# Optimization experiments

Measured on AMD Instinct MI355X. Metric: run time of the kernel, lower is better.

## Reference

```python
import jax, jax.numpy as jnp
import numpy as np

N, E, D, L, G = 50000, 640000, 128, 5, 128
BN_EPS = 1e-5

def _bn(x, g, b):
    # training-mode batchnorm over axis 0, biased variance (torch semantics)
    m = x.mean(axis=0)
    v = x.var(axis=0)
    return (x - m) * jax.lax.rsqrt(v + BN_EPS) * g + b

def setup_inputs():
    key = jax.random.key(0)
    ks = iter(jax.random.split(key, 40))
    rn = lambda shape, s=0.05: jax.random.normal(next(ks), shape, jnp.float32) * s
    inp = {}
    inp['x'] = jax.random.randint(next(ks), (N, 1), 0, 300)
    inp['edge_index'] = jax.random.randint(next(ks), (2, E), 0, N)
    inp['edge_attr'] = jax.random.normal(next(ks), (E, 7), jnp.float32)
    inp['batch'] = jnp.sort(jax.random.randint(next(ks), (N,), 0, G))
    inp['node_emb'] = rn((300, D))
    inp['vn_emb'] = jnp.zeros((1, D), jnp.float32)
    inp['eps'] = jnp.zeros((L,), jnp.float32)
    inp['edge_W'] = rn((L, 7, D)); inp['edge_b'] = rn((L, D))
    inp['W1'] = rn((L, D, 2 * D)); inp['b1'] = rn((L, 2 * D))
    inp['bn1_g'] = 1.0 + rn((L, 2 * D)); inp['bn1_b'] = rn((L, 2 * D))
    inp['W2'] = rn((L, 2 * D, D)); inp['b2'] = rn((L, D))
    inp['bn_g'] = 1.0 + rn((L, D)); inp['bn_b'] = rn((L, D))
    inp['vn_W1'] = rn((L - 1, D, 2 * D)); inp['vn_b1'] = rn((L - 1, 2 * D))
    inp['vn_bn1_g'] = 1.0 + rn((L - 1, 2 * D)); inp['vn_bn1_b'] = rn((L - 1, 2 * D))
    inp['vn_W2'] = rn((L - 1, 2 * D, D)); inp['vn_b2'] = rn((L - 1, D))
    inp['vn_bn2_g'] = 1.0 + rn((L - 1, D)); inp['vn_bn2_b'] = rn((L - 1, D))
    return inp

def reference(x, edge_index, edge_attr, batch, node_emb, vn_emb, eps,
              edge_W, edge_b, W1, b1, bn1_g, bn1_b, W2, b2, bn_g, bn_b,
              vn_W1, vn_b1, vn_bn1_g, vn_bn1_b, vn_W2, vn_b2, vn_bn2_g, vn_bn2_b):
    src, dst = edge_index[0], edge_index[1]
    h = node_emb[x[:, 0]]                      # [N, D]
    vn = jnp.broadcast_to(vn_emb, (G, D))      # virtualnode state per graph
    for l in range(L):
        h_in = h + vn[batch]                   # virtualnode broadcast
        e = edge_attr @ edge_W[l] + edge_b[l]  # [E, D]
        msg = jax.nn.relu(h_in[src] + e)       # gather + fused elementwise
        agg = jax.ops.segment_sum(msg, dst, num_segments=N)
        z = (1.0 + eps[l]) * h_in + agg
        z = jax.nn.relu(_bn(z @ W1[l] + b1[l], bn1_g[l], bn1_b[l]))
        z = _bn(z @ W2[l] + b2[l], bn_g[l], bn_b[l])
        h_out = jax.nn.relu(z) if l != L - 1 else z
        if l < L - 1:
            pooled = jax.ops.segment_sum(h_in, batch, num_segments=G)
            v = vn + pooled
            v = jax.nn.relu(_bn(v @ vn_W1[l] + vn_b1[l], vn_bn1_g[l], vn_bn1_b[l]))
            vn = jax.nn.relu(_bn(v @ vn_W2[l] + vn_b2[l], vn_bn2_g[l], vn_bn2_b[l]))
        h = h_out
    return h
```

## Files before the change

### kernel.cpp

```cpp
#include <hip/hip_runtime.h>
#include <stdint.h>

#define NN 50000
#define EE 640000
#define DD 128
#define LL 5
#define GG 128
#define D2 256

using bf16x8 = __attribute__((ext_vector_type(8))) short;
using f32x4v = __attribute__((ext_vector_type(4))) float;
using u32x4v = __attribute__((ext_vector_type(4))) unsigned int;

__device__ __forceinline__ unsigned short f2bf(float f){
  union { float f; uint32_t u; } c; c.f = f;
  uint32_t u = c.u;
  uint32_t r = (u + 0x7FFFu + ((u >> 16) & 1u)) >> 16;
  return (unsigned short)r;
}


__global__ __launch_bounds__(256) void zero_kernel(float* p, int n){
  int i = blockIdx.x*256 + threadIdx.x;
  if (i < n) p[i] = 0.f;
}

__global__ __launch_bounds__(256) void count_kernel(const int* __restrict__ ei, int* __restrict__ counts){
  int e = blockIdx.x*256 + threadIdx.x;
  if (e < EE) atomicAdd(&counts[ei[EE + e]], 1);
}

#define SCAN_B 512
__global__ __launch_bounds__(SCAN_B) void scan1_kernel(const int* __restrict__ counts, int* __restrict__ bsums, int n){
  __shared__ int sh[SCAN_B];
  int b = blockIdx.x, t = threadIdx.x;
  int i = b*SCAN_B + t;
  sh[t] = (i < n) ? counts[i] : 0;
  __syncthreads();
  for (int s = SCAN_B/2; s > 0; s >>= 1){
    if (t < s) sh[t] += sh[t+s];
    __syncthreads();
  }
  if (t == 0) bsums[b] = sh[0];
}

__global__ void scan2_kernel(int* bsums, int nb){
  if (threadIdx.x == 0){
    int run = 0;
    for (int i = 0; i < nb; ++i){ int v = bsums[i]; bsums[i] = run; run += v; }
  }
}

__global__ __launch_bounds__(SCAN_B) void scan3_kernel(const int* __restrict__ counts, const int* __restrict__ bsums,
                                                       int* __restrict__ startp, int* __restrict__ cursor, int n){
  __shared__ int sh[SCAN_B];
  int b = blockIdx.x, t = threadIdx.x;
  int i = b*SCAN_B + t;
  int v = (i < n) ? counts[i] : 0;
  sh[t] = v;
  __syncthreads();
  for (int s = 1; s < SCAN_B; s <<= 1){
    int add = (t >= s) ? sh[t-s] : 0;
    __syncthreads();
    sh[t] += add;
    __syncthreads();
  }
  int excl = sh[t] - v + bsums[b];
  if (i < n){ startp[i] = excl; cursor[i] = excl; }
  if (i == n-1) startp[n] = excl + v;
}

__global__ __launch_bounds__(256) void fill_kernel(const int* __restrict__ ei, int* __restrict__ cursor, int* __restrict__ csr){
  int e = blockIdx.x*256 + threadIdx.x;
  if (e < EE){
    int d = ei[EE + e];
    int slot = atomicAdd(&cursor[d], 1);
    csr[slot] = e;
  }
}

__global__ __launch_bounds__(256) void embed_kernel(const int* __restrict__ x, const float* __restrict__ emb, float* __restrict__ h){
  int idx = blockIdx.x*256 + threadIdx.x;
  if (idx >= NN*32) return;
  int i = idx >> 5, c4 = idx & 31;
  int xi = x[i];
  *(f32x4v*)(h + (size_t)idx*4) = *(const f32x4v*)(emb + ((size_t)xi*32 + c4)*4);
}

__global__ __launch_bounds__(256) void vninit_kernel(const float* __restrict__ vn_emb, float* __restrict__ vn){
  int idx = blockIdx.x*256 + threadIdx.x;
  if (idx >= GG*32) return;
  *(f32x4v*)(vn + (size_t)idx*4) = *(const f32x4v*)(vn_emb + (size_t)(idx & 31)*4);
}

__global__ __launch_bounds__(256) void wtrans_kernel(const float* __restrict__ W1, const float* __restrict__ W2,
                                                     unsigned short* __restrict__ W1T, unsigned short* __restrict__ W2T){
  int idx = blockIdx.x*256 + threadIdx.x;
  const int total = LL*DD*D2;
  if (idx < total){
    int l = idx / (DD*D2);
    int rem = idx - l*(DD*D2);
    int k = rem / D2;
    int c = rem - k*D2;
    W1T[(size_t)l*32768 + (size_t)c*128 + k] = f2bf(W1[idx]);
  } else if (idx < 2*total){
    int j = idx - total;
    int l = j / (DD*D2);
    int rem = j - l*(DD*D2);
    int k = rem / DD;
    int c = rem - k*DD;
    W2T[(size_t)l*32768 + (size_t)c*256 + k] = f2bf(W2[j]);
  }
}


__global__ __launch_bounds__(256) void hin_kernel(const float* __restrict__ h, const float* __restrict__ vn,
                                                  const int* __restrict__ batch, float* __restrict__ hin){
  int idx = blockIdx.x*256 + threadIdx.x;
  if (idx >= NN*32) return;
  int i = idx >> 5, c4 = idx & 31;
  int b = batch[i];
  f32x4v hv = *(const f32x4v*)(h + (size_t)idx*4);
  f32x4v vv = *(const f32x4v*)(vn + ((size_t)b*32 + c4)*4);
  *(f32x4v*)(hin + (size_t)idx*4) = hv + vv;
}

__global__ __launch_bounds__(128) void agg_kernel(const float* __restrict__ hin, const int* __restrict__ csr,
                                                  const int* __restrict__ startp, const int* __restrict__ ei,
                                                  const float* __restrict__ ea, const float* __restrict__ eW,
                                                  const float* __restrict__ eb, const float* __restrict__ eps, int l,
                                                  unsigned short* __restrict__ zout){
  int node = blockIdx.x, d = threadIdx.x;
  int s0 = startp[node], s1 = startp[node+1];
  float w[7];
  #pragma unroll
  for (int k = 0; k < 7; ++k) w[k] = eW[k*128 + d];
  float bd = eb[d];
  float acc = 0.f;
  __shared__ int eids[32];
  __shared__ int srcs[32];
  __shared__ float eav[32][8];
  for (int base = s0; base < s1; base += 32){
    int cnt = min(32, s1 - base);
    __syncthreads();
    if (d < cnt){ int e = csr[base + d]; eids[d] = e; srcs[d] = ei[e]; }
    __syncthreads();
    for (int q = d; q < cnt*7; q += 128){
      int j = q / 7, k = q - j*7;
      eav[j][k] = ea[(size_t)eids[j]*7 + k];
    }
    __syncthreads();
    for (int j = 0; j < cnt; ++j){
      float hv = hin[(size_t)srcs[j]*128 + d];
      float e = bd;
      #pragma unroll
      for (int k = 0; k < 7; ++k) e += eav[j][k]*w[k];
      float m = hv + e;
      acc += (m > 0.f) ? m : 0.f;
    }
  }
  float one = 1.f + eps[l];
  float z = one*hin[(size_t)node*128 + d] + acc;
  zout[(size_t)node*128 + d] = f2bf(z);
}

__global__ __launch_bounds__(256) void gemm1_kernel(const unsigned short* __restrict__ A,
                                                    const unsigned short* __restrict__ BT,
                                                    const float* __restrict__ bias,
                                                    float* __restrict__ Y,
                                                    float* __restrict__ sums, float* __restrict__ sqs){
  __shared__ __align__(16) unsigned short Al[128*128];
  __shared__ __align__(16) unsigned short Bl[128*128];
  const int t = threadIdx.x;
  const int rb = blockIdx.x, cb = blockIdx.y;
  for (int it = 0; it < 8; ++it){
    int idx = it*256 + t;
    int row = idx >> 4, ch = idx & 15;
    int grow = rb*128 + row;
    u32x4v v = {0,0,0,0};
    if (grow < NN) v = *(const u32x4v*)(A + (size_t)grow*128 + ch*8);
    *(u32x4v*)((char*)Al + row*256 + ((ch*16) ^ ((row&7)<<4))) = v;
  }
  for (int it = 0; it < 8; ++it){
    int idx = it*256 + t;
    int row = idx >> 4, ch = idx & 15;
    u32x4v v = *(const u32x4v*)(BT + (size_t)(cb*128 + row)*128 + ch*8);
    *(u32x4v*)((char*)Bl + row*256 + ((ch*16) ^ ((row&7)<<4))) = v;
  }
  __syncthreads();
  const int lane = t & 63, wave = t >> 6;
  const int wm = wave >> 1, wn = wave & 1;
  const int r0 = lane & 15, kg = lane >> 4;
  f32x4v acc[4][4] = {};
  #pragma unroll
  for (int kk = 0; kk < 4; ++kk){
    const int kb = kk*64 + kg*16;
    bf16x8 a[4], b[4];
    #pragma unroll
    for (int m = 0; m < 4; ++m){
      int row = wm*64 + m*16 + r0;
      a[m] = *(const bf16x8*)((const char*)Al + row*256 + (kb ^ ((r0&7)<<4)));
    }
    #pragma unroll
    for (int n = 0; n < 4; ++n){
      int col = wn*64 + n*16 + r0;
      b[n] = *(const bf16x8*)((const char*)Bl + col*256 + (kb ^ ((r0&7)<<4)));
    }
    #pragma unroll
    for (int m = 0; m < 4; ++m)
      #pragma unroll
      for (int n = 0; n < 4; ++n)
        acc[m][n] = __builtin_amdgcn_mfma_f32_16x16x32_bf16(a[m], b[n], acc[m][n], 0, 0, 0);
  }
  #pragma unroll
  for (int n = 0; n < 4; ++n){
    const int col = cb*128 + wn*64 + n*16 + r0;
    const float bv = bias[col];
    float s = 0.f, q = 0.f;
    #pragma unroll
    for (int m = 0; m < 4; ++m){
      const int rowb = rb*128 + wm*64 + m*16 + kg*4;
      #pragma unroll
      for (int j = 0; j < 4; ++j){
        int grow = rowb + j;
        if (grow < NN){
          float v = acc[m][n][j] + bv;
          Y[(size_t)grow*256 + col] = v;
          s += v; q += v*v;
        }
      }
    }
    s += __shfl_xor(s, 16); q += __shfl_xor(q, 16);
    s += __shfl_xor(s, 32); q += __shfl_xor(q, 32);
    if (kg == 0){ atomicAdd(&sums[col], s); atomicAdd(&sqs[col], q); }
  }
}

__global__ __launch_bounds__(256) void gemm2_kernel(const float* __restrict__ Yin,
                                                    const float* __restrict__ scl, const float* __restrict__ shf,
                                                    const unsigned short* __restrict__ BT,
                                                    const float* __restrict__ bias,
                                                    float* __restrict__ Y,
                                                    float* __restrict__ sums, float* __restrict__ sqs){
  __shared__ __align__(16) unsigned short Al[128*128];
  __shared__ __align__(16) unsigned short Bl[128*128];
  __shared__ float s_scl[256], s_shf[256];
  const int t = threadIdx.x;
  const int rb = blockIdx.x;
  if (t < 256){ s_scl[t] = scl[t]; s_shf[t] = shf[t]; }
  const int lane = t & 63, wave = t >> 6;
  const int wm = wave >> 1, wn = wave & 1;
  const int r0 = lane & 15, kg = lane >> 4;
  f32x4v acc[4][4] = {};
  for (int kt = 0; kt < 2; ++kt){
    __syncthreads();
    for (int it = 0; it < 8; ++it){
      int idx = it*256 + t;
      int row = idx >> 4, ch = idx & 15;
      int grow = rb*128 + row;
      int c0 = kt*128 + ch*8;
      u32x4v pv = {0,0,0,0};
      if (grow < NN){
        f32x4v ya = *(const f32x4v*)(Yin + (size_t)grow*256 + c0);
        f32x4v yb = *(const f32x4v*)(Yin + (size_t)grow*256 + c0 + 4);
        unsigned short tb[8];
        #pragma unroll
        for (int jj = 0; jj < 4; ++jj){
          float a = ya[jj]*s_scl[c0+jj] + s_shf[c0+jj];
          tb[jj] = f2bf(a > 0.f ? a : 0.f);
        }
        #pragma unroll
        for (int jj = 0; jj < 4; ++jj){
          float a = yb[jj]*s_scl[c0+4+jj] + s_shf[c0+4+jj];
          tb[4+jj] = f2bf(a > 0.f ? a : 0.f);
        }
        pv[0] = (uint32_t)tb[0] | ((uint32_t)tb[1] << 16);
        pv[1] = (uint32_t)tb[2] | ((uint32_t)tb[3] << 16);
        pv[2] = (uint32_t)tb[4] | ((uint32_t)tb[5] << 16);
        pv[3] = (uint32_t)tb[6] | ((uint32_t)tb[7] << 16);
      }
      *(u32x4v*)((char*)Al + row*256 + ((ch*16) ^ ((row&7)<<4))) = pv;
    }
    for (int it = 0; it < 8; ++it){
      int idx = it*256 + t;
      int row = idx >> 4, ch = idx & 15;
      u32x4v v = *(const u32x4v*)(BT + (size_t)row*256 + kt*128 + ch*8);
      *(u32x4v*)((char*)Bl + row*256 + ((ch*16) ^ ((row&7)<<4))) = v;
    }
    __syncthreads();
    #pragma unroll
    for (int kk = 0; kk < 4; ++kk){
      const int kb = kk*64 + kg*16;
      bf16x8 a[4], b[4];
      #pragma unroll
      for (int m = 0; m < 4; ++m){
        int row = wm*64 + m*16 + r0;
        a[m] = *(const bf16x8*)((const char*)Al + row*256 + (kb ^ ((r0&7)<<4)));
      }
      #pragma unroll
      for (int n = 0; n < 4; ++n){
        int col = wn*64 + n*16 + r0;
        b[n] = *(const bf16x8*)((const char*)Bl + col*256 + (kb ^ ((r0&7)<<4)));
      }
      #pragma unroll
      for (int m = 0; m < 4; ++m)
        #pragma unroll
        for (int n = 0; n < 4; ++n)
          acc[m][n] = __builtin_amdgcn_mfma_f32_16x16x32_bf16(a[m], b[n], acc[m][n], 0, 0, 0);
    }
  }
  #pragma unroll
  for (int n = 0; n < 4; ++n){
    const int col = wn*64 + n*16 + r0;
    const float bv = bias[col];
    float s = 0.f, q = 0.f;
    #pragma unroll
    for (int m = 0; m < 4; ++m){
      const int rowb = rb*128 + wm*64 + m*16 + kg*4;
      #pragma unroll
      for (int j = 0; j < 4; ++j){
        int grow = rowb + j;
        if (grow < NN){
          float v = acc[m][n][j] + bv;
          Y[(size_t)grow*128 + col] = v;
          s += v; q += v*v;
        }
      }
    }
    s += __shfl_xor(s, 16); q += __shfl_xor(q, 16);
    s += __shfl_xor(s, 32); q += __shfl_xor(q, 32);
    if (kg == 0){ atomicAdd(&sums[col], s); atomicAdd(&sqs[col], q); }
  }
}

__global__ void bnfin_kernel(const float* __restrict__ sums, const float* __restrict__ sqs,
                             const float* __restrict__ g, const float* __restrict__ b,
                             float* __restrict__ scl, float* __restrict__ shf, int C, float invcnt){
  int c = blockIdx.x*blockDim.x + threadIdx.x;
  if (c < C){
    float m = sums[c]*invcnt;
    float v = sqs[c]*invcnt - m*m;
    v = v > 0.f ? v : 0.f;
    float inv = rsqrtf(v + 1e-5f);
    float s = g[c]*inv;
    scl[c] = s;
    shf[c] = b[c] - m*s;
  }
}

__global__ __launch_bounds__(256) void happly_kernel(const float* __restrict__ y2, const float* __restrict__ scl,
                                                     const float* __restrict__ shf, float* __restrict__ h, int relu){
  int idx = blockIdx.x*256 + threadIdx.x;
  if (idx >= NN*32) return;
  int c4 = idx & 31;
  f32x4v y = *(const f32x4v*)(y2 + (size_t)idx*4);
  f32x4v s = *(const f32x4v*)(scl + (size_t)c4*4);
  f32x4v t = *(const f32x4v*)(shf + (size_t)c4*4);
  f32x4v o;
  #pragma unroll
  for (int j = 0; j < 4; ++j){
    float v = y[j]*s[j] + t[j];
    o[j] = (relu && v < 0.f) ? 0.f : v;
  }
  *(f32x4v*)(h + (size_t)idx*4) = o;
}

__global__ __launch_bounds__(256) void vcopy_kernel(const float* __restrict__ vn, float* __restrict__ vbuf){
  int idx = blockIdx.x*256 + threadIdx.x;
  if (idx < GG*DD) vbuf[idx] = vn[idx];
}

#define POOL_ROWS 128
__global__ __launch_bounds__(128) void pool2_kernel(const float* __restrict__ hin, const int* __restrict__ batch,
                                                    float* __restrict__ vout){
  int r0 = blockIdx.x*POOL_ROWS;
  int r1 = r0 + POOL_ROWS; if (r1 > NN) r1 = NN;
  int d = threadIdx.x;
  __shared__ int sb[POOL_ROWS];
  if (r0 + d < r1) sb[d] = batch[r0 + d];
  __syncthreads();
  int curg = sb[0];
  float acc = 0.f;
  for (int r = r0; r < r1; ++r){
    int g = sb[r - r0];
    if (g != curg){
      atomicAdd(&vout[(size_t)curg*DD + d], acc);
      acc = 0.f; curg = g;
    }
    acc += hin[(size_t)r*DD + d];
  }
  atomicAdd(&vout[(size_t)curg*DD + d], acc);
}

__global__ __launch_bounds__(256) void vmlp1_kernel(const float* __restrict__ V, const float* __restrict__ W,
                                                    const float* __restrict__ bias, float* __restrict__ Yo,
                                                    float* __restrict__ sums, float* __restrict__ sqs){
  __shared__ float vrow[128];
  int r = blockIdx.x, c = threadIdx.x;
  if (c < 128) vrow[c] = V[r*128 + c];
  __syncthreads();
  float acc = 0.f;
  #pragma unroll 8
  for (int k = 0; k < 128; ++k) acc += vrow[k]*W[k*256 + c];
  float y = acc + bias[c];
  Yo[r*256 + c] = y;
  atomicAdd(&sums[c], y);
  atomicAdd(&sqs[c], y*y);
}

__global__ __launch_bounds__(128) void vmlp2_kernel(const float* __restrict__ Yin, const float* __restrict__ scl,
                                                    const float* __restrict__ shf, const float* __restrict__ W,
                                                    const float* __restrict__ bias, float* __restrict__ Yo,
                                                    float* __restrict__ sums, float* __restrict__ sqs){
  __shared__ float arow[256];
  int r = blockIdx.x, c = threadIdx.x;
  for (int k = c; k < 256; k += 128){
    float a = Yin[r*256 + k]*scl[k] + shf[k];
    arow[k] = a > 0.f ? a : 0.f;
  }
  __syncthreads();
  float acc = 0.f;
  #pragma unroll 8
  for (int k = 0; k < 256; ++k) acc += arow[k]*W[k*128 + c];
  float y = acc + bias[c];
  Yo[r*128 + c] = y;
  atomicAdd(&sums[c], y);
  atomicAdd(&sqs[c], y*y);
}

__global__ __launch_bounds__(256) void va_kernel(const float* __restrict__ yv2, const float* __restrict__ scl,
                                                 const float* __restrict__ shf, float* __restrict__ vn){
  int idx = blockIdx.x*256 + threadIdx.x;
  if (idx < GG*128){
    int c = idx & 127;
    float v = yv2[idx]*scl[c] + shf[c];
    vn[idx] = v > 0.f ? v : 0.f;
  }
}


extern "C" void kernel_launch(void* const* d_in, const int* in_sizes, int n_in,
                              void* d_out, int out_size, void* d_ws, size_t ws_size,
                              hipStream_t stream){
  const int*   x         = (const int*)  d_in[0];
  const int*   ei        = (const int*)  d_in[1];
  const float* edge_attr = (const float*)d_in[2];
  const int*   batch     = (const int*)  d_in[3];
  const float* node_emb  = (const float*)d_in[4];
  const float* vn_emb    = (const float*)d_in[5];
  const float* eps       = (const float*)d_in[6];
  const float* edge_W    = (const float*)d_in[7];
  const float* edge_b    = (const float*)d_in[8];
  const float* W1        = (const float*)d_in[9];
  const float* b1        = (const float*)d_in[10];
  const float* bn1_g     = (const float*)d_in[11];
  const float* bn1_b     = (const float*)d_in[12];
  const float* W2        = (const float*)d_in[13];
  const float* b2        = (const float*)d_in[14];
  const float* bn_g      = (const float*)d_in[15];
  const float* bn_b      = (const float*)d_in[16];
  const float* vn_W1     = (const float*)d_in[17];
  const float* vn_b1     = (const float*)d_in[18];
  const float* vn_bn1_g  = (const float*)d_in[19];
  const float* vn_bn1_b  = (const float*)d_in[20];
  const float* vn_W2     = (const float*)d_in[21];
  const float* vn_b2     = (const float*)d_in[22];
  const float* vn_bn2_g  = (const float*)d_in[23];
  const float* vn_bn2_b  = (const float*)d_in[24];
  float* h = (float*)d_out;

  char* ws = (char*)d_ws;
  size_t off = 0;
  auto alloc = [&](size_t bytes)->char*{
    char* p = ws + off; off += (bytes + 255) & ~(size_t)255; return p;
  };
  float*          hin    = (float*)         alloc((size_t)NN*DD*4);
  float*          y1     = (float*)         alloc((size_t)NN*D2*4);
  float*          y2     = (float*)         alloc((size_t)NN*DD*4);
  unsigned short* zbuf   = (unsigned short*)alloc((size_t)NN*DD*2);
  float*          vn     = (float*)         alloc((size_t)GG*DD*4);
  float*          vbuf   = (float*)         alloc((size_t)GG*DD*4);
  float*          yv1    = (float*)         alloc((size_t)GG*D2*4);
  float*          yv2    = (float*)         alloc((size_t)GG*DD*4);
  unsigned short* W1T    = (unsigned short*)alloc((size_t)LL*D2*DD*2);
  unsigned short* W2T    = (unsigned short*)alloc((size_t)LL*D2*DD*2);
  float*          stats  = (float*)         alloc(16*256*4);
  int*            counts = (int*)           alloc((size_t)NN*4);
  int*            startp = (int*)           alloc((size_t)(NN+1)*4);
  int*            cursor = (int*)           alloc((size_t)NN*4);
  int*            csr    = (int*)           alloc((size_t)EE*4);
  int*            bsums  = (int*)           alloc(128*4);

  float* sum1 = stats + 0*256,  *sq1 = stats + 1*256,  *scale1 = stats + 2*256,  *shift1 = stats + 3*256;
  float* sum2 = stats + 4*256,  *sq2 = stats + 5*256,  *scale2 = stats + 6*256,  *shift2 = stats + 7*256;
  float* sumv1= stats + 8*256,  *sqv1= stats + 9*256,  *scalev1= stats + 10*256, *shiftv1= stats + 11*256;
  float* sumv2= stats + 12*256, *sqv2= stats + 13*256, *scalev2= stats + 14*256, *shiftv2= stats + 15*256;

  const int nb_scan = (NN + SCAN_B - 1)/SCAN_B;
  const int ew_blocks = (NN*32 + 255)/256;
  const int pool_blocks = (NN + POOL_ROWS - 1)/POOL_ROWS;

  zero_kernel<<<(NN+255)/256, 256, 0, stream>>>((float*)counts, NN);
  count_kernel<<<EE/256, 256, 0, stream>>>(ei, counts);
  scan1_kernel<<<nb_scan, SCAN_B, 0, stream>>>(counts, bsums, NN);
  scan2_kernel<<<1, 64, 0, stream>>>(bsums, nb_scan);
  scan3_kernel<<<nb_scan, SCAN_B, 0, stream>>>(counts, bsums, startp, cursor, NN);
  fill_kernel<<<EE/256, 256, 0, stream>>>(ei, cursor, csr);
  embed_kernel<<<ew_blocks, 256, 0, stream>>>(x, node_emb, h);
  vninit_kernel<<<(GG*32 + 255)/256, 256, 0, stream>>>(vn_emb, vn);
  wtrans_kernel<<<(2*LL*DD*D2 + 255)/256, 256, 0, stream>>>(W1, W2, W1T, W2T);

  for (int l = 0; l < LL; ++l){
    zero_kernel<<<16, 256, 0, stream>>>(stats, 16*256);
    hin_kernel<<<ew_blocks, 256, 0, stream>>>(h, vn, batch, hin);
    agg_kernel<<<NN, 128, 0, stream>>>(hin, csr, startp, ei, edge_attr,
                                       edge_W + (size_t)l*7*DD, edge_b + (size_t)l*DD, eps, l, zbuf);
    gemm1_kernel<<<dim3((NN+127)/128, 2), 256, 0, stream>>>(zbuf, W1T + (size_t)l*32768,
                                                            b1 + (size_t)l*D2, y1, sum1, sq1);
    bnfin_kernel<<<1, 256, 0, stream>>>(sum1, sq1, bn1_g + (size_t)l*D2, bn1_b + (size_t)l*D2,
                                        scale1, shift1, D2, 1.f/(float)NN);
    gemm2_kernel<<<(NN+127)/128, 256, 0, stream>>>(y1, scale1, shift1, W2T + (size_t)l*32768,
                                                   b2 + (size_t)l*DD, y2, sum2, sq2);
    bnfin_kernel<<<1, 256, 0, stream>>>(sum2, sq2, bn_g + (size_t)l*DD, bn_b + (size_t)l*DD,
                                        scale2, shift2, DD, 1.f/(float)NN);
    happly_kernel<<<ew_blocks, 256, 0, stream>>>(y2, scale2, shift2, h, (l != LL-1) ? 1 : 0);
    if (l < LL-1){
      vcopy_kernel<<<(GG*DD + 255)/256, 256, 0, stream>>>(vn, vbuf);
      pool2_kernel<<<pool_blocks, 128, 0, stream>>>(hin, batch, vbuf);
      vmlp1_kernel<<<GG, 256, 0, stream>>>(vbuf, vn_W1 + (size_t)l*DD*D2, vn_b1 + (size_t)l*D2,
                                           yv1, sumv1, sqv1);
      bnfin_kernel<<<1, 256, 0, stream>>>(sumv1, sqv1, vn_bn1_g + (size_t)l*D2, vn_bn1_b + (size_t)l*D2,
                                          scalev1, shiftv1, D2, 1.f/(float)GG);
      vmlp2_kernel<<<GG, 128, 0, stream>>>(yv1, scalev1, shiftv1, vn_W2 + (size_t)l*D2*DD,
                                           vn_b2 + (size_t)l*DD, yv2, sumv2, sqv2);
      bnfin_kernel<<<1, 256, 0, stream>>>(sumv2, sqv2, vn_bn2_g + (size_t)l*DD, vn_bn2_b + (size_t)l*DD,
                                          scalev2, shiftv2, DD, 1.f/(float)GG);
      va_kernel<<<(GG*DD + 255)/256, 256, 0, stream>>>(yv2, scalev2, shiftv2, vn);
    }
  }
  (void)in_sizes; (void)n_in; (void)out_size; (void)ws_size;
}
```

Baseline: 1.374 ms.

## Fuse layer epilogues, store activations in bf16, and presort edge data by destination

Pre-gathers edge sources and padded edge attributes into destination-sorted CSR order so aggregation reads them contiguously. Node states and intermediate activations (hin, y1, y2) are stored in bf16 instead of fp32, roughly halving traffic in gather, GEMM and elementwise passes. Batchnorm finalisation is folded into consumer kernels, and the h-apply, virtual-node add and pooling steps are fused into one per-layer kernel, with per-layer stats zeroed once up front. This cuts kernel launches and memory passes at the cost of extra bf16 rounding and a reordering of when the virtual node is updated relative to pooling.

```diff
diff --git a/kernel.cpp b/kernel.cpp
--- a/kernel.cpp
+++ b/kernel.cpp
@@ -17,6 +17,9 @@
   uint32_t u = c.u;
   uint32_t r = (u + 0x7FFFu + ((u >> 16) & 1u)) >> 16;
   return (unsigned short)r;
+}
+__device__ __forceinline__ float bf2f(unsigned short u){
+  union { uint32_t u; float f; } c; c.u = ((uint32_t)u) << 16; return c.f;
 }
 
 
@@ -79,18 +82,20 @@
   }
 }
 
-__global__ __launch_bounds__(256) void embed_kernel(const int* __restrict__ x, const float* __restrict__ emb, float* __restrict__ h){
-  int idx = blockIdx.x*256 + threadIdx.x;
-  if (idx >= NN*32) return;
-  int i = idx >> 5, c4 = idx & 31;
-  int xi = x[i];
-  *(f32x4v*)(h + (size_t)idx*4) = *(const f32x4v*)(emb + ((size_t)xi*32 + c4)*4);
-}
-
-__global__ __launch_bounds__(256) void vninit_kernel(const float* __restrict__ vn_emb, float* __restrict__ vn){
-  int idx = blockIdx.x*256 + threadIdx.x;
-  if (idx >= GG*32) return;
-  *(f32x4v*)(vn + (size_t)idx*4) = *(const f32x4v*)(vn_emb + (size_t)(idx & 31)*4);
+__global__ __launch_bounds__(256) void egather_kernel(const int* __restrict__ csr, const int* __restrict__ ei,
+                                                      const float* __restrict__ ea,
+                                                      int* __restrict__ csr_src, float* __restrict__ csr_ea8){
+  int s = blockIdx.x*256 + threadIdx.x;
+  if (s < EE){
+    int e = csr[s];
+    csr_src[s] = ei[e];
+    float v[8];
+    #pragma unroll
+    for (int k = 0; k < 7; ++k) v[k] = ea[(size_t)e*7 + k];
+    v[7] = 0.f;
+    #pragma unroll
+    for (int k = 0; k < 8; ++k) csr_ea8[(size_t)s*8 + k] = v[k];
+  }
 }
 
 __global__ __launch_bounds__(256) void wtrans_kernel(const float* __restrict__ W1, const float* __restrict__ W2,
@@ -113,23 +118,43 @@
   }
 }
 
-
-__global__ __launch_bounds__(256) void hin_kernel(const float* __restrict__ h, const float* __restrict__ vn,
-                                                  const int* __restrict__ batch, float* __restrict__ hin){
-  int idx = blockIdx.x*256 + threadIdx.x;
-  if (idx >= NN*32) return;
-  int i = idx >> 5, c4 = idx & 31;
-  int b = batch[i];
-  f32x4v hv = *(const f32x4v*)(h + (size_t)idx*4);
-  f32x4v vv = *(const f32x4v*)(vn + ((size_t)b*32 + c4)*4);
-  *(f32x4v*)(hin + (size_t)idx*4) = hv + vv;
-}
-
-__global__ __launch_bounds__(128) void agg_kernel(const float* __restrict__ hin, const int* __restrict__ csr,
-                                                  const int* __restrict__ startp, const int* __restrict__ ei,
-                                                  const float* __restrict__ ea, const float* __restrict__ eW,
-                                                  const float* __restrict__ eb, const float* __restrict__ eps, int l,
-                                                  unsigned short* __restrict__ zout){
+__global__ __launch_bounds__(128) void init_kernel(const int* __restrict__ x, const int* __restrict__ batch,
+                                                   const float* __restrict__ emb, const float* __restrict__ vn_emb,
+                                                   unsigned short* __restrict__ hin_bf, float* __restrict__ vbuf0,
+                                                   float* __restrict__ vn){
+  int r0 = blockIdx.x*128;
+  int r1 = r0 + 128; if (r1 > NN) r1 = NN;
+  int d = threadIdx.x;
+  float ve = vn_emb[d];
+  if (blockIdx.x == 0){
+    for (int g = 0; g < GG; ++g) vn[(size_t)g*DD + d] = ve;
+  }
+  __shared__ int sb[128];
+  __shared__ int sx[128];
+  if (r0 + d < r1){ sb[d] = batch[r0 + d]; sx[d] = x[r0 + d]; }
+  __syncthreads();
+  int curg = sb[0];
+  float pacc = 0.f;
+  for (int r = r0; r < r1; ++r){
+    int g = sb[r - r0];
+    if (g != curg){
+      atomicAdd(&vbuf0[(size_t)curg*DD + d], pacc);
+      pacc = 0.f; curg = g;
+    }
+    float hv = emb[(size_t)sx[r - r0]*DD + d] + ve;
+    hin_bf[(size_t)r*DD + d] = f2bf(hv);
+    pacc += hv;
+  }
+  atomicAdd(&vbuf0[(size_t)curg*DD + d], pacc);
+}
+
+
+__global__ __launch_bounds__(128) void agg2_kernel(const unsigned short* __restrict__ hin_bf,
+                                                   const int* __restrict__ csr_src, const float* __restrict__ csr_ea8,
+                                                   const int* __restrict__ startp,
+                                                   const float* __restrict__ eW, const float* __restrict__ eb,
+                                                   const float* __restrict__ eps, int l,
+                                                   unsigned short* __restrict__ zout){
   int node = blockIdx.x, d = threadIdx.x;
   int s0 = startp[node], s1 = startp[node+1];
   float w[7];
@@ -137,37 +162,34 @@
   for (int k = 0; k < 7; ++k) w[k] = eW[k*128 + d];
   float bd = eb[d];
   float acc = 0.f;
-  __shared__ int eids[32];
-  __shared__ int srcs[32];
-  __shared__ float eav[32][8];
+  __shared__ int ssrc[32];
+  __shared__ float sattr[32][8];
   for (int base = s0; base < s1; base += 32){
     int cnt = min(32, s1 - base);
     __syncthreads();
-    if (d < cnt){ int e = csr[base + d]; eids[d] = e; srcs[d] = ei[e]; }
-    __syncthreads();
-    for (int q = d; q < cnt*7; q += 128){
-      int j = q / 7, k = q - j*7;
-      eav[j][k] = ea[(size_t)eids[j]*7 + k];
+    if (d < cnt) ssrc[d] = csr_src[base + d];
+    for (int q = d; q < cnt*8; q += 128){
+      sattr[q >> 3][q & 7] = csr_ea8[(size_t)base*8 + q];
     }
     __syncthreads();
     for (int j = 0; j < cnt; ++j){
-      float hv = hin[(size_t)srcs[j]*128 + d];
+      float hv = bf2f(hin_bf[(size_t)ssrc[j]*128 + d]);
       float e = bd;
       #pragma unroll
-      for (int k = 0; k < 7; ++k) e += eav[j][k]*w[k];
+      for (int k = 0; k < 7; ++k) e += sattr[j][k]*w[k];
       float m = hv + e;
       acc += (m > 0.f) ? m : 0.f;
     }
   }
   float one = 1.f + eps[l];
-  float z = one*hin[(size_t)node*128 + d] + acc;
+  float z = one*bf2f(hin_bf[(size_t)node*128 + d]) + acc;
   zout[(size_t)node*128 + d] = f2bf(z);
 }
 
 __global__ __launch_bounds__(256) void gemm1_kernel(const unsigned short* __restrict__ A,
                                                     const unsigned short* __restrict__ BT,
                                                     const float* __restrict__ bias,
-                                                    float* __restrict__ Y,
+                                                    unsigned short* __restrict__ Y,
                                                     float* __restrict__ sums, float* __restrict__ sqs){
   __shared__ __align__(16) unsigned short Al[128*128];
   __shared__ __align__(16) unsigned short Bl[128*128];
@@ -225,7 +247,7 @@
         int grow = rowb + j;
         if (grow < NN){
           float v = acc[m][n][j] + bv;
-          Y[(size_t)grow*256 + col] = v;
+          Y[(size_t)grow*256 + col] = f2bf(v);
           s += v; q += v*v;
         }
       }
@@ -236,18 +258,28 @@
   }
 }
 
-__global__ __launch_bounds__(256) void gemm2_kernel(const float* __restrict__ Yin,
-                                                    const float* __restrict__ scl, const float* __restrict__ shf,
+template<int FINAL>
+__global__ __launch_bounds__(256) void gemm2_kernel(const unsigned short* __restrict__ Yin,
+                                                    const float* __restrict__ sum1, const float* __restrict__ sq1,
+                                                    const float* __restrict__ bg, const float* __restrict__ bb,
                                                     const unsigned short* __restrict__ BT,
                                                     const float* __restrict__ bias,
-                                                    float* __restrict__ Y,
+                                                    unsigned short* __restrict__ Yh, float* __restrict__ Yf,
                                                     float* __restrict__ sums, float* __restrict__ sqs){
   __shared__ __align__(16) unsigned short Al[128*128];
   __shared__ __align__(16) unsigned short Bl[128*128];
   __shared__ float s_scl[256], s_shf[256];
   const int t = threadIdx.x;
   const int rb = blockIdx.x;
-  if (t < 256){ s_scl[t] = scl[t]; s_shf[t] = shf[t]; }
+  {
+    const float invn = 1.f/(float)NN;
+    float m = sum1[t]*invn;
+    float var = sq1[t]*invn - m*m;
+    var = var > 0.f ? var : 0.f;
+    float sc = bg[t]*rsqrtf(var + 1e-5f);
+    s_scl[t] = sc;
+    s_shf[t] = bb[t] - m*sc;
+  }
   const int lane = t & 63, wave = t >> 6;
   const int wm = wave >> 1, wn = wave & 1;
   const int r0 = lane & 15, kg = lane >> 4;
@@ -261,18 +293,17 @@
       int c0 = kt*128 + ch*8;
       u32x4v pv = {0,0,0,0};
       if (grow < NN){
-        f32x4v ya = *(const f32x4v*)(Yin + (size_t)grow*256 + c0);
-        f32x4v yb = *(const f32x4v*)(Yin + (size_t)grow*256 + c0 + 4);
+        u32x4v yv = *(const u32x4v*)(Yin + (size_t)grow*256 + c0);
         unsigned short tb[8];
         #pragma unroll
         for (int jj = 0; jj < 4; ++jj){
-          float a = ya[jj]*s_scl[c0+jj] + s_shf[c0+jj];
-          tb[jj] = f2bf(a > 0.f ? a : 0.f);
-        }
-        #pragma unroll
-        for (int jj = 0; jj < 4; ++jj){
-          float a = yb[jj]*s_scl[c0+4+jj] + s_shf[c0+4+jj];
-          tb[4+jj] = f2bf(a > 0.f ? a : 0.f);
+          uint32_t pw = yv[jj];
+          float a0 = bf2f((unsigned short)(pw & 0xFFFFu));
+          float a1 = bf2f((unsigned short)(pw >> 16));
+          float v0 = a0*s_scl[c0 + 2*jj]     + s_shf[c0 + 2*jj];
+          float v1 = a1*s_scl[c0 + 2*jj + 1] + s_shf[c0 + 2*jj + 1];
+          tb[2*jj]     = f2bf(v0 > 0.f ? v0 : 0.f);
+          tb[2*jj + 1] = f2bf(v1 > 0.f ? v1 : 0.f);
         }
         pv[0] = (uint32_t)tb[0] | ((uint32_t)tb[1] << 16);
         pv[1] = (uint32_t)tb[2] | ((uint32_t)tb[3] << 16);
@@ -322,7 +353,8 @@
         int grow = rowb + j;
         if (grow < NN){
           float v = acc[m][n][j] + bv;
-          Y[(size_t)grow*128 + col] = v;
+          if (FINAL) Yf[(size_t)grow*128 + col] = v;
+          else       Yh[(size_t)grow*128 + col] = f2bf(v);
           s += v; q += v*v;
         }
       }
@@ -333,71 +365,71 @@
   }
 }
 
-__global__ void bnfin_kernel(const float* __restrict__ sums, const float* __restrict__ sqs,
-                             const float* __restrict__ g, const float* __restrict__ b,
-                             float* __restrict__ scl, float* __restrict__ shf, int C, float invcnt){
-  int c = blockIdx.x*blockDim.x + threadIdx.x;
-  if (c < C){
-    float m = sums[c]*invcnt;
-    float v = sqs[c]*invcnt - m*m;
+__global__ __launch_bounds__(128) void happly_fused_kernel(const unsigned short* __restrict__ y2h,
+                                                           const float* __restrict__ sum2, const float* __restrict__ sq2,
+                                                           const float* __restrict__ bg, const float* __restrict__ bb,
+                                                           const float* __restrict__ vn, const int* __restrict__ batch,
+                                                           unsigned short* __restrict__ hin_bf, float* __restrict__ vbuf_next){
+  int r0 = blockIdx.x*128;
+  int r1 = r0 + 128; if (r1 > NN) r1 = NN;
+  int d = threadIdx.x;
+  const float invn = 1.f/(float)NN;
+  float m = sum2[d]*invn;
+  float var = sq2[d]*invn - m*m;
+  var = var > 0.f ? var : 0.f;
+  float sc = bg[d]*rsqrtf(var + 1e-5f);
+  float sh = bb[d] - m*sc;
+  __shared__ int sb[128];
+  if (r0 + d < r1) sb[d] = batch[r0 + d];
+  __syncthreads();
+  int curg = sb[0];
+  float vnv = vn[(size_t)curg*DD + d];
+  float pacc = 0.f;
+  for (int r = r0; r < r1; ++r){
+    int g = sb[r - r0];
+    if (g != curg){
+      atomicAdd(&vbuf_next[(size_t)curg*DD + d], pacc);
+      pacc = 0.f; curg = g;
+      vnv = vn[(size_t)curg*DD + d];
+    }
+    float y = bf2f(y2h[(size_t)r*DD + d]);
+    float v = y*sc + sh;
     v = v > 0.f ? v : 0.f;
-    float inv = rsqrtf(v + 1e-5f);
-    float s = g[c]*inv;
-    scl[c] = s;
-    shf[c] = b[c] - m*s;
-  }
-}
-
-__global__ __launch_bounds__(256) void happly_kernel(const float* __restrict__ y2, const float* __restrict__ scl,
-                                                     const float* __restrict__ shf, float* __restrict__ h, int relu){
+    float hv = v + vnv;
+    hin_bf[(size_t)r*DD + d] = f2bf(hv);
+    pacc += hv;
+  }
+  atomicAdd(&vbuf_next[(size_t)curg*DD + d], pacc);
+}
+
+__global__ __launch_bounds__(256) void happly_final_kernel(float* __restrict__ y,
+                                                           const float* __restrict__ sum2, const float* __restrict__ sq2,
+                                                           const float* __restrict__ bg, const float* __restrict__ bb){
   int idx = blockIdx.x*256 + threadIdx.x;
   if (idx >= NN*32) return;
   int c4 = idx & 31;
-  f32x4v y = *(const f32x4v*)(y2 + (size_t)idx*4);
-  f32x4v s = *(const f32x4v*)(scl + (size_t)c4*4);
-  f32x4v t = *(const f32x4v*)(shf + (size_t)c4*4);
+  const float invn = 1.f/(float)NN;
+  f32x4v yv = *(const f32x4v*)(y + (size_t)idx*4);
   f32x4v o;
   #pragma unroll
   for (int j = 0; j < 4; ++j){
-    float v = y[j]*s[j] + t[j];
-    o[j] = (relu && v < 0.f) ? 0.f : v;
-  }
-  *(f32x4v*)(h + (size_t)idx*4) = o;
-}
-
-__global__ __launch_bounds__(256) void vcopy_kernel(const float* __restrict__ vn, float* __restrict__ vbuf){
-  int idx = blockIdx.x*256 + threadIdx.x;
-  if (idx < GG*DD) vbuf[idx] = vn[idx];
-}
-
-#define POOL_ROWS 128
-__global__ __launch_bounds__(128) void pool2_kernel(const float* __restrict__ hin, const int* __restrict__ batch,
-                                                    float* __restrict__ vout){
-  int r0 = blockIdx.x*POOL_ROWS;
-  int r1 = r0 + POOL_ROWS; if (r1 > NN) r1 = NN;
-  int d = threadIdx.x;
-  __shared__ int sb[POOL_ROWS];
-  if (r0 + d < r1) sb[d] = batch[r0 + d];
-  __syncthreads();
-  int curg = sb[0];
-  float acc = 0.f;
-  for (int r = r0; r < r1; ++r){
-    int g = sb[r - r0];
-    if (g != curg){
-      atomicAdd(&vout[(size_t)curg*DD + d], acc);
-      acc = 0.f; curg = g;
-    }
-    acc += hin[(size_t)r*DD + d];
-  }
-  atomicAdd(&vout[(size_t)curg*DD + d], acc);
-}
-
-__global__ __launch_bounds__(256) void vmlp1_kernel(const float* __restrict__ V, const float* __restrict__ W,
-                                                    const float* __restrict__ bias, float* __restrict__ Yo,
+    int c = c4*4 + j;
+    float m = sum2[c]*invn;
+    float var = sq2[c]*invn - m*m;
+    var = var > 0.f ? var : 0.f;
+    float sc = bg[c]*rsqrtf(var + 1e-5f);
+    o[j] = (yv[j] - m)*sc + bb[c];
+  }
+  *(f32x4v*)(y + (size_t)idx*4) = o;
+}
+
+__global__ __launch_bounds__(256) void vmlp1_kernel(const float* __restrict__ vn, const float* __restrict__ vbufl,
+                                                    const float* __restrict__ W, const float* __restrict__ bias,
+                                                    float* __restrict__ Yo,
                                                     float* __restrict__ sums, float* __restrict__ sqs){
   __shared__ float vrow[128];
   int r = blockIdx.x, c = threadIdx.x;
-  if (c < 128) vrow[c] = V[r*128 + c];
+  if (c < 128) vrow[c] = vn[r*128 + c] + vbufl[r*128 + c];
   __syncthreads();
   float acc = 0.f;
   #pragma unroll 8
@@ -408,14 +440,27 @@
   atomicAdd(&sqs[c], y*y);
 }
 
-__global__ __launch_bounds__(128) void vmlp2_kernel(const float* __restrict__ Yin, const float* __restrict__ scl,
-                                                    const float* __restrict__ shf, const float* __restrict__ W,
-                                                    const float* __restrict__ bias, float* __restrict__ Yo,
+__global__ __launch_bounds__(128) void vmlp2_kernel(const float* __restrict__ Yin,
+                                                    const float* __restrict__ sumv1, const float* __restrict__ sqv1,
+                                                    const float* __restrict__ vg, const float* __restrict__ vb,
+                                                    const float* __restrict__ W, const float* __restrict__ bias,
+                                                    float* __restrict__ Yo,
                                                     float* __restrict__ sums, float* __restrict__ sqs){
   __shared__ float arow[256];
+  __shared__ float s_scl[256], s_shf[256];
   int r = blockIdx.x, c = threadIdx.x;
+  const float invg = 1.f/(float)GG;
   for (int k = c; k < 256; k += 128){
-    float a = Yin[r*256 + k]*scl[k] + shf[k];
+    float m = sumv1[k]*invg;
+    float var = sqv1[k]*invg - m*m;
+    var = var > 0.f ? var : 0.f;
+    float sc = vg[k]*rsqrtf(var + 1e-5f);
+    s_scl[k] = sc;
+    s_shf[k] = vb[k] - m*sc;
+  }
+  __syncthreads();
+  for (int k = c; k < 256; k += 128){
+    float a = Yin[r*256 + k]*s_scl[k] + s_shf[k];
     arow[k] = a > 0.f ? a : 0.f;
   }
   __syncthreads();
@@ -428,12 +473,19 @@
   atomicAdd(&sqs[c], y*y);
 }
 
-__global__ __launch_bounds__(256) void va_kernel(const float* __restrict__ yv2, const float* __restrict__ scl,
-                                                 const float* __restrict__ shf, float* __restrict__ vn){
+__global__ __launch_bounds__(256) void va_kernel(const float* __restrict__ yv2,
+                                                 const float* __restrict__ sumv2, const float* __restrict__ sqv2,
+                                                 const float* __restrict__ vg, const float* __restrict__ vb,
+                                                 float* __restrict__ vn){
   int idx = blockIdx.x*256 + threadIdx.x;
   if (idx < GG*128){
     int c = idx & 127;
-    float v = yv2[idx]*scl[c] + shf[c];
+    const float invg = 1.f/(float)GG;
+    float m = sumv2[c]*invg;
+    float var = sqv2[c]*invg - m*m;
+    var = var > 0.f ? var : 0.f;
+    float sc = vg[c]*rsqrtf(var + 1e-5f);
+    float v = (yv2[idx] - m)*sc + vb[c];
     vn[idx] = v > 0.f ? v : 0.f;
   }
 }
@@ -467,75 +519,85 @@
   const float* vn_b2     = (const float*)d_in[22];
   const float* vn_bn2_g  = (const float*)d_in[23];
   const float* vn_bn2_b  = (const float*)d_in[24];
-  float* h = (float*)d_out;
+  float* hout = (float*)d_out;
 
   char* ws = (char*)d_ws;
   size_t off = 0;
   auto alloc = [&](size_t bytes)->char*{
     char* p = ws + off; off += (bytes + 255) & ~(size_t)255; return p;
   };
-  float*          hin    = (float*)         alloc((size_t)NN*DD*4);
-  float*          y1     = (float*)         alloc((size_t)NN*D2*4);
-  float*          y2     = (float*)         alloc((size_t)NN*DD*4);
-  unsigned short* zbuf   = (unsigned short*)alloc((size_t)NN*DD*2);
+  unsigned short* hin_bf = (unsigned short*)alloc((size_t)NN*DD*2);
+  unsigned short* zy     = (unsigned short*)alloc((size_t)NN*DD*2);
+  unsigned short* y1h    = (unsigned short*)alloc((size_t)NN*D2*2);
   float*          vn     = (float*)         alloc((size_t)GG*DD*4);
-  float*          vbuf   = (float*)         alloc((size_t)GG*DD*4);
   float*          yv1    = (float*)         alloc((size_t)GG*D2*4);
   float*          yv2    = (float*)         alloc((size_t)GG*DD*4);
   unsigned short* W1T    = (unsigned short*)alloc((size_t)LL*D2*DD*2);
   unsigned short* W2T    = (unsigned short*)alloc((size_t)LL*D2*DD*2);
-  float*          stats  = (float*)         alloc(16*256*4);
-  int*            counts = (int*)           alloc((size_t)NN*4);
-  int*            startp = (int*)           alloc((size_t)(NN+1)*4);
-  int*            cursor = (int*)           alloc((size_t)NN*4);
-  int*            csr    = (int*)           alloc((size_t)EE*4);
-  int*            bsums  = (int*)           alloc(128*4);
-
-  float* sum1 = stats + 0*256,  *sq1 = stats + 1*256,  *scale1 = stats + 2*256,  *shift1 = stats + 3*256;
-  float* sum2 = stats + 4*256,  *sq2 = stats + 5*256,  *scale2 = stats + 6*256,  *shift2 = stats + 7*256;
-  float* sumv1= stats + 8*256,  *sqv1= stats + 9*256,  *scalev1= stats + 10*256, *shiftv1= stats + 11*256;
-  float* sumv2= stats + 12*256, *sqv2= stats + 13*256, *scalev2= stats + 14*256, *shiftv2= stats + 15*256;
+  const int STATS_F = LL*8*256;
+  const int VBUF_F  = 5*GG*DD;
+  const int ZTOT    = STATS_F + VBUF_F + NN;
+  float* zeroreg = (float*)alloc((size_t)ZTOT*4);
+  float* stats_all = zeroreg;
+  float* vbuf_all  = zeroreg + STATS_F;
+  int*   counts    = (int*)(zeroreg + STATS_F + VBUF_F);
+  int*   startp = (int*)  alloc((size_t)(NN+1)*4);
+  int*   cursor = (int*)  alloc((size_t)NN*4);
+  int*   csr    = (int*)  alloc((size_t)EE*4);
+  int*   bsums  = (int*)  alloc(128*4);
+  int*   csr_src= (int*)  alloc((size_t)EE*4);
+  float* csr_ea8= (float*)alloc((size_t)EE*8*4);
 
   const int nb_scan = (NN + SCAN_B - 1)/SCAN_B;
+  const int row_blocks = (NN + 127)/128;
   const int ew_blocks = (NN*32 + 255)/256;
-  const int pool_blocks = (NN + POOL_ROWS - 1)/POOL_ROWS;
-
-  zero_kernel<<<(NN+255)/256, 256, 0, stream>>>((float*)counts, NN);
+
+  zero_kernel<<<(ZTOT + 255)/256, 256, 0, stream>>>(zeroreg, ZTOT);
   count_kernel<<<EE/256, 256, 0, stream>>>(ei, counts);
   scan1_kernel<<<nb_scan, SCAN_B, 0, stream>>>(counts, bsums, NN);
   scan2_kernel<<<1, 64, 0, stream>>>(bsums, nb_scan);
   scan3_kernel<<<nb_scan, SCAN_B, 0, stream>>>(counts, bsums, startp, cursor, NN);
   fill_kernel<<<EE/256, 256, 0, stream>>>(ei, cursor, csr);
-  embed_kernel<<<ew_blocks, 256, 0, stream>>>(x, node_emb, h);
-  vninit_kernel<<<(GG*32 + 255)/256, 256, 0, stream>>>(vn_emb, vn);
+  egather_kernel<<<EE/256, 256, 0, stream>>>(csr, ei, edge_attr, csr_src, csr_ea8);
   wtrans_kernel<<<(2*LL*DD*D2 + 255)/256, 256, 0, stream>>>(W1, W2, W1T, W2T);
+  init_kernel<<<row_blocks, 128, 0, stream>>>(x, batch, node_emb, vn_emb, hin_bf, vbuf_all, vn);
 
   for (int l = 0; l < LL; ++l){
-    zero_kernel<<<16, 256, 0, stream>>>(stats, 16*256);
-    hin_kernel<<<ew_blocks, 256, 0, stream>>>(h, vn, batch, hin);
-    agg_kernel<<<NN, 128, 0, stream>>>(hin, csr, startp, ei, edge_attr,
-                                       edge_W + (size_t)l*7*DD, edge_b + (size_t)l*DD, eps, l, zbuf);
-    gemm1_kernel<<<dim3((NN+127)/128, 2), 256, 0, stream>>>(zbuf, W1T + (size_t)l*32768,
-                                                            b1 + (size_t)l*D2, y1, sum1, sq1);
-    bnfin_kernel<<<1, 256, 0, stream>>>(sum1, sq1, bn1_g + (size_t)l*D2, bn1_b + (size_t)l*D2,
-                                        scale1, shift1, D2, 1.f/(float)NN);
-    gemm2_kernel<<<(NN+127)/128, 256, 0, stream>>>(y1, scale1, shift1, W2T + (size_t)l*32768,
-                                                   b2 + (size_t)l*DD, y2, sum2, sq2);
-    bnfin_kernel<<<1, 256, 0, stream>>>(sum2, sq2, bn_g + (size_t)l*DD, bn_b + (size_t)l*DD,
-                                        scale2, shift2, DD, 1.f/(float)NN);
-    happly_kernel<<<ew_blocks, 256, 0, stream>>>(y2, scale2, shift2, h, (l != LL-1) ? 1 : 0);
-    if (l < LL-1){
-      vcopy_kernel<<<(GG*DD + 255)/256, 256, 0, stream>>>(vn, vbuf);
-      pool2_kernel<<<pool_blocks, 128, 0, stream>>>(hin, batch, vbuf);
-      vmlp1_kernel<<<GG, 256, 0, stream>>>(vbuf, vn_W1 + (size_t)l*DD*D2, vn_b1 + (size_t)l*D2,
+    float* st    = stats_all + (size_t)l*8*256;
+    float* sum1  = st + 0*256, *sq1  = st + 1*256;
+    float* sum2  = st + 2*256, *sq2  = st + 3*256;
+    float* sumv1 = st + 4*256, *sqv1 = st + 5*256;
+    float* sumv2 = st + 6*256, *sqv2 = st + 7*256;
+
+    agg2_kernel<<<NN, 128, 0, stream>>>(hin_bf, csr_src, csr_ea8, startp,
+                                        edge_W + (size_t)l*7*DD, edge_b + (size_t)l*DD, eps, l, zy);
+    gemm1_kernel<<<dim3(row_blocks, 2), 256, 0, stream>>>(zy, W1T + (size_t)l*32768,
+                                                          b1 + (size_t)l*D2, y1h, sum1, sq1);
+    if (l != LL-1){
+      gemm2_kernel<0><<<row_blocks, 256, 0, stream>>>(y1h, sum1, sq1,
+                                                      bn1_g + (size_t)l*D2, bn1_b + (size_t)l*D2,
+                                                      W2T + (size_t)l*32768, b2 + (size_t)l*DD,
+                                                      zy, nullptr, sum2, sq2);
+      float* vbufl = vbuf_all + (size_t)l*GG*DD;
+      float* vbufn = vbuf_all + (size_t)(l+1)*GG*DD;
+      vmlp1_kernel<<<GG, 256, 0, stream>>>(vn, vbufl, vn_W1 + (size_t)l*DD*D2, vn_b1 + (size_t)l*D2,
                                            yv1, sumv1, sqv1);
-      bnfin_kernel<<<1, 256, 0, stream>>>(sumv1, sqv1, vn_bn1_g + (size_t)l*D2, vn_bn1_b + (size_t)l*D2,
-                                          scalev1, shiftv1, D2, 1.f/(float)GG);
-      vmlp2_kernel<<<GG, 128, 0, stream>>>(yv1, scalev1, shiftv1, vn_W2 + (size_t)l*D2*DD,
-                                           vn_b2 + (size_t)l*DD, yv2, sumv2, sqv2);
-      bnfin_kernel<<<1, 256, 0, stream>>>(sumv2, sqv2, vn_bn2_g + (size_t)l*DD, vn_bn2_b + (size_t)l*DD,
-                                          scalev2, shiftv2, DD, 1.f/(float)GG);
-      va_kernel<<<(GG*DD + 255)/256, 256, 0, stream>>>(yv2, scalev2, shiftv2, vn);
+      vmlp2_kernel<<<GG, 128, 0, stream>>>(yv1, sumv1, sqv1,
+                                           vn_bn1_g + (size_t)l*D2, vn_bn1_b + (size_t)l*D2,
+                                           vn_W2 + (size_t)l*D2*DD, vn_b2 + (size_t)l*DD,
+                                           yv2, sumv2, sqv2);
+      va_kernel<<<(GG*DD + 255)/256, 256, 0, stream>>>(yv2, sumv2, sqv2,
+                                                       vn_bn2_g + (size_t)l*DD, vn_bn2_b + (size_t)l*DD, vn);
+      happly_fused_kernel<<<row_blocks, 128, 0, stream>>>(zy, sum2, sq2,
+                                                          bn_g + (size_t)l*DD, bn_b + (size_t)l*DD,
+                                                          vn, batch, hin_bf, vbufn);
+    } else {
+      gemm2_kernel<1><<<row_blocks, 256, 0, stream>>>(y1h, sum1, sq1,
+                                                      bn1_g + (size_t)l*D2, bn1_b + (size_t)l*D2,
+                                                      W2T + (size_t)l*32768, b2 + (size_t)l*DD,
+                                                      nullptr, hout, sum2, sq2);
+      happly_final_kernel<<<ew_blocks, 256, 0, stream>>>(hout, sum2, sq2,
+                                                         bn_g + (size_t)l*DD, bn_b + (size_t)l*DD);
     }
   }
   (void)in_sizes; (void)n_in; (void)out_size; (void)ws_size;
```

Result: faster. 1.263 ms (-8.1%).
